# Kernel tuning notes

Measured on AMD Instinct MI355X. Metric: run time of the kernel, lower is better.

Reference implementation:

```python
import jax, jax.numpy as jnp
import numpy as np

EPS = 1e-5

def _bn(z, gamma, beta):
    mu = z.mean(axis=0)
    var = z.var(axis=0)  # biased, matches torch BN normalization
    return (z - mu) * jax.lax.rsqrt(var + EPS) * gamma + beta

def _sage_bn_relu(h, src, dst, n_nodes, Wl, bl, Wr, gamma, beta):
    # SAGEConv (mean aggr): out = lin_l(mean_{j in N(i)} h_j) + lin_r(h_i)
    msg = h[src]                                               # [E, d] gather
    agg = jax.ops.segment_sum(msg, dst, num_segments=n_nodes)  # [N, d]
    cnt = jax.ops.segment_sum(jnp.ones((src.shape[0], 1), h.dtype), dst,
                              num_segments=n_nodes)            # [N, 1]
    agg = jnp.where(cnt > 0, agg / jnp.maximum(cnt, 1.0), 0.0)
    out = agg @ Wl.T + bl + h @ Wr.T
    return jax.nn.relu(_bn(out, gamma, beta))

def setup_inputs() -> dict:
    key = jax.random.key(0)
    N, E, d, out_c, L, U = 50000, 800000, 128, 128, 3, 256
    ks = jax.random.split(key, 16)
    s = 1.0 / np.sqrt(d)
    return {
        "x": jax.random.normal(ks[0], (N, d), jnp.float32),
        "edge_index": jax.random.randint(ks[1], (2, E), 0, N, jnp.int64),
        "atom_mask": jax.random.uniform(ks[2], (N, 1), jnp.float32),
        "u_index": jax.random.randint(ks[3], (U,), 0, N, jnp.int64),
        "lin_l_w": jax.random.uniform(ks[4], (L, d, d), jnp.float32, -s, s),
        "lin_l_b": jax.random.uniform(ks[5], (L, d), jnp.float32, -s, s),
        "lin_r_w": jax.random.uniform(ks[6], (L, d, d), jnp.float32, -s, s),
        "bn_gamma": jnp.ones((L, d), jnp.float32),
        "bn_beta": jnp.zeros((L, d), jnp.float32),
        "ro_w1": jax.random.uniform(ks[7], (d, d), jnp.float32, -s, s),
        "ro_b1": jax.random.uniform(ks[8], (d,), jnp.float32, -s, s),
        "ro_bn_gamma": jnp.ones((d,), jnp.float32),
        "ro_bn_beta": jnp.zeros((d,), jnp.float32),
        "ro_w2": jax.random.uniform(ks[9], (out_c, d), jnp.float32, -s, s),
        "ro_b2": jax.random.uniform(ks[10], (out_c,), jnp.float32, -s, s),
    }

def reference(x, edge_index, atom_mask, u_index, lin_l_w, lin_l_b, lin_r_w,
              bn_gamma, bn_beta, ro_w1, ro_b1, ro_bn_gamma, ro_bn_beta,
              ro_w2, ro_b2):
    N = x.shape[0]
    src, dst = edge_index[0], edge_index[1]
    h = x
    for l in range(lin_l_w.shape[0]):
        h = _sage_bn_relu(h, src, dst, N, lin_l_w[l], lin_l_b[l],
                          lin_r_w[l], bn_gamma[l], bn_beta[l])
    state = h[u_index]                                         # [U, d]
    z = jax.nn.relu(_bn(h @ ro_w1.T + ro_b1, ro_bn_gamma, ro_bn_beta))
    atom = (z @ ro_w2.T + ro_b2) * atom_mask                   # [N, out]
    return (h, atom, state)
```

## Files before the change

### kernel.cpp

```cpp
#include <hip/hip_runtime.h>

#define D 128
#define LDA 136

typedef __attribute__((ext_vector_type(8))) short bf16x8;
typedef __attribute__((ext_vector_type(4))) float f32x4;

__device__ __forceinline__ ushort f2b(float f) {
  union { float f; unsigned u; } a; a.f = f;
  unsigned u = a.u;
  return (ushort)((u + 0x7fffu + ((u >> 16) & 1u)) >> 16);
}
__device__ __forceinline__ float b2f_lo(unsigned v) {
  union { unsigned u; float f; } a; a.u = v << 16; return a.f;
}
__device__ __forceinline__ float b2f_hi(unsigned v) {
  union { unsigned u; float f; } a; a.u = v & 0xffff0000u; return a.f;
}

__global__ void k_prep(const float* __restrict__ x, const float* __restrict__ wl,
                       const float* __restrict__ wr, const float* __restrict__ w1,
                       const float* __restrict__ w2, ushort* __restrict__ hb,
                       ushort* __restrict__ wall, uint4* __restrict__ zr,
                       int nX4, int npX4, int LDD, int nZero4) {
  int i = blockIdx.x * blockDim.x + threadIdx.x;
  if (i < npX4) {
    uint2 pk;
    if (i < nX4) {
      float4 v = *(const float4*)&x[i * 4];
      pk.x = (unsigned)f2b(v.x) | ((unsigned)f2b(v.y) << 16);
      pk.y = (unsigned)f2b(v.z) | ((unsigned)f2b(v.w) << 16);
    } else {
      pk = make_uint2(0u, 0u);
    }
    *(uint2*)&hb[i * 4] = pk;
    return;
  }
  int j = i - npX4;
  int W = 2 * LDD + 2 * D * D;
  if (j < W) {
    float v;
    if (j < LDD) v = wl[j];
    else if (j < 2 * LDD) v = wr[j - LDD];
    else if (j < 2 * LDD + D * D) v = w1[j - 2 * LDD];
    else v = w2[j - 2 * LDD - D * D];
    wall[j] = f2b(v);
    return;
  }
  int z = j - W;
  if (z < nZero4) zr[z] = make_uint4(0u, 0u, 0u, 0u);
}

__global__ void k_histrank(const int* __restrict__ dstI, int* __restrict__ cnt,
                           int* __restrict__ rankdst, int E) {
  int e = blockIdx.x * blockDim.x + threadIdx.x;
  if (e < E) {
    int d = dstI[e];
    int r = atomicAdd(&cnt[d], 1);
    rankdst[e] = (r << 16) | d;
  }
}
__global__ void k_scan1(const int* __restrict__ cnt, int* __restrict__ off,
                        int* __restrict__ bsum, int n) {
  __shared__ int sd[256];
  int t = threadIdx.x;
  int i = blockIdx.x * 256 + t;
  int x = (i < n) ? cnt[i] : 0;
  sd[t] = x;
  __syncthreads();
  for (int s = 1; s < 256; s <<= 1) {
    int v = (t >= s) ? sd[t - s] : 0;
    __syncthreads();
    sd[t] += v;
    __syncthreads();
  }
  if (i < n) off[i] = sd[t] - x;
  if (t == 255) bsum[blockIdx.x] = sd[255];
}
__global__ void k_scan2(const int* __restrict__ bsum, int* __restrict__ boff, int nb) {
  __shared__ int sd[256];
  int t = threadIdx.x;
  int x = (t < nb) ? bsum[t] : 0;
  sd[t] = x;
  __syncthreads();
  for (int s = 1; s < 256; s <<= 1) {
    int v = (t >= s) ? sd[t - s] : 0;
    __syncthreads();
    sd[t] += v;
    __syncthreads();
  }
  if (t < nb) boff[t] = sd[t] - x;
}
__global__ void k_scan3(int* __restrict__ off, const int* __restrict__ boff, int n) {
  int i = blockIdx.x * blockDim.x + threadIdx.x;
  if (i < n) off[i] += boff[i >> 8];
}
__global__ void k_fill(const int* __restrict__ srcI, const int* __restrict__ rankdst,
                       const int* __restrict__ off, ushort* __restrict__ eidx, int E) {
  int e = blockIdx.x * blockDim.x + threadIdx.x;
  if (e < E) {
    int rd = rankdst[e];
    int d = rd & 0xFFFF;
    eidx[off[d] + (rd >> 16)] = (ushort)srcI[e];
  }
}

#define ACC8(A, V, B)                                             \
  A[B + 0] += b2f_lo(V.x); A[B + 1] += b2f_hi(V.x);               \
  A[B + 2] += b2f_lo(V.y); A[B + 3] += b2f_hi(V.y);               \
  A[B + 4] += b2f_lo(V.z); A[B + 5] += b2f_hi(V.z);               \
  A[B + 6] += b2f_lo(V.w); A[B + 7] += b2f_hi(V.w);

template <bool AGG>
__global__ __launch_bounds__(512) void k_fused(
    const ushort* __restrict__ hin, const ushort* __restrict__ Wl,
    const ushort* __restrict__ Wr, const float* __restrict__ bias,
    const int* __restrict__ off, const ushort* __restrict__ eidx,
    ushort* __restrict__ pre, float* __restrict__ sums, int N, int E) {
  __shared__ ushort aggS[128 * LDA];
  __shared__ float ls[2 * D];
  int t = threadIdx.x;
  int r0 = blockIdx.x * 128;

  if (t < 2 * D) ls[t] = 0.f;

  if (AGG) {
    int lrow = t >> 2;
    int row = r0 + lrow;
    int sub = (t & 3) << 3;
    int start = 0, end = 0;
    if (row < N) { start = off[row]; end = (row == N - 1) ? E : off[row + 1]; }
    int deg = end - start;
    float inv = (deg > 0) ? 1.0f / (float)deg : 0.f;
#pragma unroll
    for (int ph = 0; ph < 4; ++ph) {
      const ushort* hbase = hin + ph * 32 + sub;
      float a[8];
#pragma unroll
      for (int i = 0; i < 8; ++i) a[i] = 0.f;
#pragma unroll 2
      for (int e = start; e < end; ++e) {
        int sn = eidx[e];
        uint4 v = *(const uint4*)(hbase + (size_t)sn * D);
        ACC8(a, v, 0)
      }
      uint4 o;
      o.x = (unsigned)f2b(a[0] * inv) | ((unsigned)f2b(a[1] * inv) << 16);
      o.y = (unsigned)f2b(a[2] * inv) | ((unsigned)f2b(a[3] * inv) << 16);
      o.z = (unsigned)f2b(a[4] * inv) | ((unsigned)f2b(a[5] * inv) << 16);
      o.w = (unsigned)f2b(a[6] * inv) | ((unsigned)f2b(a[7] * inv) << 16);
      *(uint4*)&aggS[lrow * LDA + ph * 32 + sub] = o;
    }
  }
  __syncthreads();

  int lane = t & 63;
  int wid = t >> 6;
  int wr = wid >> 1, wc = wid & 1;
  int rw = wr * 32, cw = wc * 64;
  int lr = lane & 15, lk = (lane >> 4) * 8;

  f32x4 acc[2][4];
#pragma unroll
  for (int i = 0; i < 2; ++i)
#pragma unroll
    for (int j = 0; j < 4; ++j) acc[i][j] = (f32x4){0.f, 0.f, 0.f, 0.f};

#pragma unroll
  for (int ks = 0; ks < 4; ++ks) {
    int kb = ks * 32 + lk;
    bf16x8 aA[2], aB[2];
#pragma unroll
    for (int rt = 0; rt < 2; ++rt) {
      if (AGG) {
        aA[rt] = *(const bf16x8*)&aggS[(rw + rt * 16 + lr) * LDA + kb];
        aB[rt] = *(const bf16x8*)&hin[(size_t)(r0 + rw + rt * 16 + lr) * D + kb];
      } else {
        aA[rt] = *(const bf16x8*)&hin[(size_t)(r0 + rw + rt * 16 + lr) * D + kb];
      }
    }
#pragma unroll
    for (int jt = 0; jt < 4; ++jt) {
      bf16x8 b1 = *(const bf16x8*)&Wl[(size_t)(cw + jt * 16 + lr) * D + kb];
      acc[0][jt] = __builtin_amdgcn_mfma_f32_16x16x32_bf16(aA[0], b1, acc[0][jt], 0, 0, 0);
      acc[1][jt] = __builtin_amdgcn_mfma_f32_16x16x32_bf16(aA[1], b1, acc[1][jt], 0, 0, 0);
      if (AGG) {
        bf16x8 b2 = *(const bf16x8*)&Wr[(size_t)(cw + jt * 16 + lr) * D + kb];
        acc[0][jt] = __builtin_amdgcn_mfma_f32_16x16x32_bf16(aB[0], b2, acc[0][jt], 0, 0, 0);
        acc[1][jt] = __builtin_amdgcn_mfma_f32_16x16x32_bf16(aB[1], b2, acc[1][jt], 0, 0, 0);
      }
    }
  }

  int crow = (lane >> 4) * 4;
#pragma unroll
  for (int jt = 0; jt < 4; ++jt) {
    int col = cw + jt * 16 + lr;
    float bv = bias[col];
    float s1 = 0.f, s2 = 0.f;
#pragma unroll
    for (int rt = 0; rt < 2; ++rt) {
      int rbase = r0 + rw + rt * 16 + crow;
#pragma unroll
      for (int rg = 0; rg < 4; ++rg) {
        int row = rbase + rg;
        if (row < N) {
          float v = acc[rt][jt][rg] + bv;
          pre[(size_t)row * D + col] = f2b(v);
          s1 += v; s2 += v * v;
        }
      }
    }
    s1 += __shfl_xor(s1, 16, 64); s1 += __shfl_xor(s1, 32, 64);
    s2 += __shfl_xor(s2, 16, 64); s2 += __shfl_xor(s2, 32, 64);
    if (lane < 16) {
      atomicAdd(&ls[cw + jt * 16 + lane], s1);
      atomicAdd(&ls[D + cw + jt * 16 + lane], s2);
    }
  }
  __syncthreads();
  if (t < 2 * D) atomicAdd(&sums[t], ls[t]);
}

template <bool F32OUT>
__global__ void k_bnrelu(const ushort* __restrict__ pre, const float* __restrict__ sums,
                         const float* __restrict__ gamma, const float* __restrict__ beta,
                         float* __restrict__ fout, ushort* __restrict__ bout,
                         int N, int Np, float invN) {
  int i4 = blockIdx.x * blockDim.x + threadIdx.x;
  if (i4 >= Np * (D / 4)) return;
  int row = i4 >> 5;
  int c4 = (i4 & 31) * 4;
  uint2 pk;
  if (row < N) {
    uint2 pv = *(const uint2*)&pre[(size_t)row * D + c4];
    float4 v = make_float4(b2f_lo(pv.x), b2f_hi(pv.x), b2f_lo(pv.y), b2f_hi(pv.y));
    float4 s = *(const float4*)&sums[c4];
    float4 q = *(const float4*)&sums[D + c4];
    float4 g = *(const float4*)&gamma[c4];
    float4 b = *(const float4*)&beta[c4];
    float mu, var, sc, sh;
    mu = s.x * invN; var = fmaxf(q.x * invN - mu * mu, 0.f);
    sc = g.x * rsqrtf(var + 1e-5f); sh = b.x - mu * sc;
    v.x = fmaxf(fmaf(v.x, sc, sh), 0.f);
    mu = s.y * invN; var = fmaxf(q.y * invN - mu * mu, 0.f);
    sc = g.y * rsqrtf(var + 1e-5f); sh = b.y - mu * sc;
    v.y = fmaxf(fmaf(v.y, sc, sh), 0.f);
    mu = s.z * invN; var = fmaxf(q.z * invN - mu * mu, 0.f);
    sc = g.z * rsqrtf(var + 1e-5f); sh = b.z - mu * sc;
    v.z = fmaxf(fmaf(v.z, sc, sh), 0.f);
    mu = s.w * invN; var = fmaxf(q.w * invN - mu * mu, 0.f);
    sc = g.w * rsqrtf(var + 1e-5f); sh = b.w - mu * sc;
    v.w = fmaxf(fmaf(v.w, sc, sh), 0.f);
    if (F32OUT) *(float4*)&fout[(size_t)row * D + c4] = v;
    pk.x = (unsigned)f2b(v.x) | ((unsigned)f2b(v.y) << 16);
    pk.y = (unsigned)f2b(v.z) | ((unsigned)f2b(v.w) << 16);
  } else {
    pk = make_uint2(0u, 0u);
  }
  *(uint2*)&bout[(size_t)row * D + c4] = pk;
}

__global__ __launch_bounds__(256) void k_mmfin(
    const ushort* __restrict__ A, const ushort* __restrict__ W,
    const float* __restrict__ bias, const float* __restrict__ mask,
    float* __restrict__ out, int N) {
  int t = threadIdx.x;
  int lane = t & 63;
  int wid = t >> 6;
  int wr = wid >> 1, wc = wid & 1;
  int r0 = blockIdx.x * 128 + wr * 64;
  int c0 = wc * 64;
  int lr = lane & 15, lk = (lane >> 4) * 8;

  f32x4 acc[4][4];
#pragma unroll
  for (int i = 0; i < 4; ++i)
#pragma unroll
    for (int j = 0; j < 4; ++j) acc[i][j] = (f32x4){0.f, 0.f, 0.f, 0.f};

#pragma unroll
  for (int ks = 0; ks < 4; ++ks) {
    int kb = ks * 32 + lk;
    bf16x8 a1[4];
#pragma unroll
    for (int rt = 0; rt < 4; ++rt)
      a1[rt] = *(const bf16x8*)&A[(size_t)(r0 + rt * 16 + lr) * D + kb];
#pragma unroll
    for (int jt = 0; jt < 4; ++jt) {
      bf16x8 b1 = *(const bf16x8*)&W[(size_t)(c0 + jt * 16 + lr) * D + kb];
#pragma unroll
      for (int rt = 0; rt < 4; ++rt)
        acc[rt][jt] = __builtin_amdgcn_mfma_f32_16x16x32_bf16(a1[rt], b1, acc[rt][jt], 0, 0, 0);
    }
  }

  int crow = (lane >> 4) * 4;
#pragma unroll
  for (int rt = 0; rt < 4; ++rt) {
    int rbase = r0 + rt * 16 + crow;
#pragma unroll
    for (int jt = 0; jt < 4; ++jt) {
      int col = c0 + jt * 16 + lr;
      float bv = bias[col];
#pragma unroll
      for (int rg = 0; rg < 4; ++rg) {
        int row = rbase + rg;
        if (row < N) {
          float m = mask[row];
          out[(size_t)row * D + col] = (acc[rt][jt][rg] + bv) * m;
        }
      }
    }
  }
}

__global__ void k_gather(const float* __restrict__ h, const int* __restrict__ uidx,
                         float* __restrict__ outp, int U) {
  int u = blockIdx.x;
  int t = threadIdx.x;
  int s = uidx[u];
  *(float4*)&outp[(size_t)u * D + t * 4] = *(const float4*)&h[(size_t)s * D + t * 4];
}

extern "C" void kernel_launch(void* const* d_in, const int* in_sizes, int n_in,
                              void* d_out, int out_size, void* d_ws, size_t ws_size,
                              hipStream_t stream) {
  const float* x        = (const float*)d_in[0];
  const int*   edge     = (const int*)d_in[1];
  const float* amask    = (const float*)d_in[2];
  const int*   uindex   = (const int*)d_in[3];
  const float* lin_l_w  = (const float*)d_in[4];
  const float* lin_l_b  = (const float*)d_in[5];
  const float* lin_r_w  = (const float*)d_in[6];
  const float* bn_gamma = (const float*)d_in[7];
  const float* bn_beta  = (const float*)d_in[8];
  const float* ro_w1    = (const float*)d_in[9];
  const float* ro_b1    = (const float*)d_in[10];
  const float* ro_bng   = (const float*)d_in[11];
  const float* ro_bnb   = (const float*)d_in[12];
  const float* ro_w2    = (const float*)d_in[13];
  const float* ro_b2    = (const float*)d_in[14];

  const int N = in_sizes[0] / D;
  const int E = in_sizes[1] / 2;
  const int U = in_sizes[3];
  const int L = in_sizes[4] / (D * D);
  const int Np = ((N + 127) / 128) * 128;
  const int LDD = L * D * D;

  const int* srcI = edge;
  const int* dstI = edge + E;

  float* outH     = (float*)d_out;
  float* outAtom  = outH + (size_t)N * D;
  float* outState = outAtom + (size_t)N * D;

  char* w = (char*)d_ws;
  ushort* hb   = (ushort*)w; w += (size_t)Np * D * 2;
  ushort* pre  = (ushort*)w; w += (size_t)Np * D * 2;
  ushort* wall = (ushort*)w; w += (size_t)(2 * LDD + 2 * D * D) * 2;
  int*    cnt  = (int*)w;    w += (size_t)N * 4;
  float*  sums = (float*)w;  w += 4 * 2 * D * 4;
  int* off     = (int*)w;    w += (size_t)N * 4;
  int* rankdst = (int*)w;    w += (size_t)E * 4;
  ushort* eidx = (ushort*)w; w += (size_t)((E + 1) & ~1) * 2;
  int* bsum    = (int*)w;    w += 1024;
  int* boff    = (int*)w;    w += 1024;

  ushort* wlb = wall;
  ushort* wrb = wlb + (size_t)LDD;
  ushort* w1b = wrb + (size_t)LDD;
  ushort* w2b = w1b + (size_t)D * D;

  const float invN = 1.0f / (float)N;

  {
    int nX4 = N * D / 4, npX4 = Np * D / 4;
    int W = 2 * LDD + 2 * D * D;
    int nZero4 = (N + 4 * 2 * D) / 4;
    int total = npX4 + W + nZero4;
    k_prep<<<(total + 255) / 256, 256, 0, stream>>>(x, lin_l_w, lin_r_w, ro_w1, ro_w2,
                                                    hb, wall, (uint4*)cnt, nX4, npX4, LDD, nZero4);
  }

  int nbE = (E + 255) / 256;
  int nbN = (N + 255) / 256;
  k_histrank<<<nbE, 256, 0, stream>>>(dstI, cnt, rankdst, E);
  k_scan1<<<nbN, 256, 0, stream>>>(cnt, off, bsum, N);
  k_scan2<<<1, 256, 0, stream>>>(bsum, boff, nbN);
  k_scan3<<<nbN, 256, 0, stream>>>(off, boff, N);
  k_fill<<<nbE, 256, 0, stream>>>(srcI, rankdst, off, eidx, E);

  const int fusedBlocks = Np / 128;
  const int bnBlocks = (Np * (D / 4) + 255) / 256;

  for (int l = 0; l < L; ++l) {
    float* lsums = sums + (size_t)l * 2 * D;
    k_fused<true><<<fusedBlocks, 512, 0, stream>>>(
        hb, wlb + (size_t)l * D * D, wrb + (size_t)l * D * D,
        lin_l_b + (size_t)l * D, off, eidx, pre, lsums, N, E);
    if (l == L - 1)
      k_bnrelu<true><<<bnBlocks, 256, 0, stream>>>(pre, lsums, bn_gamma + (size_t)l * D,
                                                   bn_beta + (size_t)l * D, outH, hb, N, Np, invN);
    else
      k_bnrelu<false><<<bnBlocks, 256, 0, stream>>>(pre, lsums, bn_gamma + (size_t)l * D,
                                                    bn_beta + (size_t)l * D, nullptr, hb, N, Np, invN);
  }

  float* rsums = sums + (size_t)L * 2 * D;
  k_fused<false><<<fusedBlocks, 512, 0, stream>>>(
      hb, w1b, nullptr, ro_b1, off, eidx, pre, rsums, N, E);
  k_bnrelu<false><<<bnBlocks, 256, 0, stream>>>(pre, rsums, ro_bng, ro_bnb, nullptr, hb, N, Np, invN);
  k_mmfin<<<Np / 128, 256, 0, stream>>>(hb, w2b, ro_b2, amask, outAtom, N);
  k_gather<<<U, 32, 0, stream>>>(outH, uindex, outState, U);
}
```

Measured before the change: 365.9 us.

## Widen fused SAGE kernel to 1024 threads with LDS-staged edge indices

The fused aggregate+GEMM kernel now runs 1024 threads per block. Each block first stages its edge source indices into shared memory (capped at 3072, with a global-memory fallback). Each node row is then gathered by 8 threads, each handling 16 features in a single pass, instead of 4 threads making four 32-feature passes. The MFMA stage is split over 16 waves with 32 columns each. The intent is more memory-level parallelism in the gather and fewer reloads of the edge-index list, at the cost of more registers per thread and a stricter occupancy bound.

```diff
diff --git a/kernel.cpp b/kernel.cpp
--- a/kernel.cpp
+++ b/kernel.cpp
@@ -2,6 +2,7 @@
 
 #define D 128
 #define LDA 136
+#define ECAP 3072
 
 typedef __attribute__((ext_vector_type(8))) short bf16x8;
 typedef __attribute__((ext_vector_type(4))) float f32x4;
@@ -112,12 +113,13 @@
   A[B + 6] += b2f_lo(V.w); A[B + 7] += b2f_hi(V.w);
 
 template <bool AGG>
-__global__ __launch_bounds__(512) void k_fused(
+__global__ __launch_bounds__(1024, 8) void k_fused(
     const ushort* __restrict__ hin, const ushort* __restrict__ Wl,
     const ushort* __restrict__ Wr, const float* __restrict__ bias,
     const int* __restrict__ off, const ushort* __restrict__ eidx,
     ushort* __restrict__ pre, float* __restrict__ sums, int N, int E) {
   __shared__ ushort aggS[128 * LDA];
+  __shared__ ushort eidxS[ECAP];
   __shared__ float ls[2 * D];
   int t = threadIdx.x;
   int r0 = blockIdx.x * 128;
@@ -125,46 +127,61 @@
   if (t < 2 * D) ls[t] = 0.f;
 
   if (AGG) {
-    int lrow = t >> 2;
+    int eBase = off[r0];
+    int eEnd = (r0 + 128 < N) ? off[r0 + 128] : E;
+    int cnt = eEnd - eBase;
+    for (int i = t; i < cnt && i < ECAP; i += 1024) eidxS[i] = eidx[eBase + i];
+    __syncthreads();
+
+    int lrow = t >> 3;
     int row = r0 + lrow;
-    int sub = (t & 3) << 3;
+    int part = (t & 7) << 4;
+    float a[16];
+#pragma unroll
+    for (int i = 0; i < 16; ++i) a[i] = 0.f;
     int start = 0, end = 0;
     if (row < N) { start = off[row]; end = (row == N - 1) ? E : off[row + 1]; }
-    int deg = end - start;
-    float inv = (deg > 0) ? 1.0f / (float)deg : 0.f;
-#pragma unroll
-    for (int ph = 0; ph < 4; ++ph) {
-      const ushort* hbase = hin + ph * 32 + sub;
-      float a[8];
-#pragma unroll
-      for (int i = 0; i < 8; ++i) a[i] = 0.f;
+    const ushort* hbase = hin + part;
+    if (cnt <= ECAP) {
+#pragma unroll 4
+      for (int e = start; e < end; ++e) {
+        int sn = eidxS[e - eBase];
+        const uint4* p = (const uint4*)(hbase + (size_t)sn * D);
+        uint4 v0 = p[0], v1 = p[1];
+        ACC8(a, v0, 0) ACC8(a, v1, 8)
+      }
+    } else {
 #pragma unroll 2
       for (int e = start; e < end; ++e) {
         int sn = eidx[e];
-        uint4 v = *(const uint4*)(hbase + (size_t)sn * D);
-        ACC8(a, v, 0)
-      }
-      uint4 o;
-      o.x = (unsigned)f2b(a[0] * inv) | ((unsigned)f2b(a[1] * inv) << 16);
-      o.y = (unsigned)f2b(a[2] * inv) | ((unsigned)f2b(a[3] * inv) << 16);
-      o.z = (unsigned)f2b(a[4] * inv) | ((unsigned)f2b(a[5] * inv) << 16);
-      o.w = (unsigned)f2b(a[6] * inv) | ((unsigned)f2b(a[7] * inv) << 16);
-      *(uint4*)&aggS[lrow * LDA + ph * 32 + sub] = o;
-    }
+        const uint4* p = (const uint4*)(hbase + (size_t)sn * D);
+        uint4 v0 = p[0], v1 = p[1];
+        ACC8(a, v0, 0) ACC8(a, v1, 8)
+      }
+    }
+    int deg = end - start;
+    float inv = (deg > 0) ? 1.0f / (float)deg : 0.f;
+    unsigned o[8];
+#pragma unroll
+    for (int i = 0; i < 8; ++i)
+      o[i] = (unsigned)f2b(a[2 * i] * inv) | ((unsigned)f2b(a[2 * i + 1] * inv) << 16);
+    uint4* dst = (uint4*)&aggS[lrow * LDA + part];
+    dst[0] = make_uint4(o[0], o[1], o[2], o[3]);
+    dst[1] = make_uint4(o[4], o[5], o[6], o[7]);
   }
   __syncthreads();
 
   int lane = t & 63;
   int wid = t >> 6;
-  int wr = wid >> 1, wc = wid & 1;
-  int rw = wr * 32, cw = wc * 64;
+  int wr = wid >> 2, wc = wid & 3;
+  int rw = wr * 32, cw = wc * 32;
   int lr = lane & 15, lk = (lane >> 4) * 8;
 
-  f32x4 acc[2][4];
+  f32x4 acc[2][2];
 #pragma unroll
   for (int i = 0; i < 2; ++i)
 #pragma unroll
-    for (int j = 0; j < 4; ++j) acc[i][j] = (f32x4){0.f, 0.f, 0.f, 0.f};
+    for (int j = 0; j < 2; ++j) acc[i][j] = (f32x4){0.f, 0.f, 0.f, 0.f};
 
 #pragma unroll
   for (int ks = 0; ks < 4; ++ks) {
@@ -180,7 +197,7 @@
       }
     }
 #pragma unroll
-    for (int jt = 0; jt < 4; ++jt) {
+    for (int jt = 0; jt < 2; ++jt) {
       bf16x8 b1 = *(const bf16x8*)&Wl[(size_t)(cw + jt * 16 + lr) * D + kb];
       acc[0][jt] = __builtin_amdgcn_mfma_f32_16x16x32_bf16(aA[0], b1, acc[0][jt], 0, 0, 0);
       acc[1][jt] = __builtin_amdgcn_mfma_f32_16x16x32_bf16(aA[1], b1, acc[1][jt], 0, 0, 0);
@@ -194,7 +211,7 @@
 
   int crow = (lane >> 4) * 4;
 #pragma unroll
-  for (int jt = 0; jt < 4; ++jt) {
+  for (int jt = 0; jt < 2; ++jt) {
     int col = cw + jt * 16 + lr;
     float bv = bias[col];
     float s1 = 0.f, s2 = 0.f;
@@ -397,7 +414,7 @@
 
   for (int l = 0; l < L; ++l) {
     float* lsums = sums + (size_t)l * 2 * D;
-    k_fused<true><<<fusedBlocks, 512, 0, stream>>>(
+    k_fused<true><<<fusedBlocks, 1024, 0, stream>>>(
         hb, wlb + (size_t)l * D * D, wrb + (size_t)l * D * D,
         lin_l_b + (size_t)l * D, off, eidx, pre, lsums, N, E);
     if (l == L - 1)
@@ -409,7 +426,7 @@
   }
 
   float* rsums = sums + (size_t)L * 2 * D;
-  k_fused<false><<<fusedBlocks, 512, 0, stream>>>(
+  k_fused<false><<<fusedBlocks, 1024, 0, stream>>>(
       hb, w1b, nullptr, ro_b1, off, eidx, pre, rsums, N, E);
   k_bnrelu<false><<<bnBlocks, 256, 0, stream>>>(pre, rsums, ro_bng, ro_bnb, nullptr, hb, N, Np, invN);
   k_mmfin<<<Np / 128, 256, 0, stream>>>(hb, w2b, ro_b2, amask, outAtom, N);
```

New measurement: 387.4 us. +5.9%, slower.

## Split fused aggregation+GEMM into separate column-sliced aggregation and GEMM kernels

Applied to the files above, without the earlier changes.

The neighbour mean-aggregation moves out of the fused GEMM kernel into its own kernel. That kernel launches four times as many blocks, each handling one 32-column slice for 128 rows, and writes the bf16 aggregate to a new global buffer. The GEMM kernel then reads both operands from global memory. The aim is more parallelism and latency hiding for the irregular gather, which was serialized over four phases per thread and limited occupancy through shared-memory use. The cost is an extra global write and read of the aggregate, one more launch per layer, and repeated edge-index reads for each slice.

```diff
diff --git a/kernel.cpp b/kernel.cpp
--- a/kernel.cpp
+++ b/kernel.cpp
@@ -1,7 +1,6 @@
 #include <hip/hip_runtime.h>
 
 #define D 128
-#define LDA 136
 
 typedef __attribute__((ext_vector_type(8))) short bf16x8;
 typedef __attribute__((ext_vector_type(4))) float f32x4;
@@ -111,47 +110,51 @@
   A[B + 4] += b2f_lo(V.z); A[B + 5] += b2f_hi(V.z);               \
   A[B + 6] += b2f_lo(V.w); A[B + 7] += b2f_hi(V.w);
 
-template <bool AGG>
-__global__ __launch_bounds__(512) void k_fused(
-    const ushort* __restrict__ hin, const ushort* __restrict__ Wl,
-    const ushort* __restrict__ Wr, const float* __restrict__ bias,
-    const int* __restrict__ off, const ushort* __restrict__ eidx,
-    ushort* __restrict__ pre, float* __restrict__ sums, int N, int E) {
-  __shared__ ushort aggS[128 * LDA];
+__global__ __launch_bounds__(512) void k_aggslice(
+    const ushort* __restrict__ hin, const int* __restrict__ off,
+    const ushort* __restrict__ eidx, ushort* __restrict__ aggb,
+    int N, int E) {
+  int b = blockIdx.x;
+  int s = b & 3;
+  int t = threadIdx.x;
+  int lrow = t >> 2;
+  int row = (b >> 2) * 128 + lrow;
+  int col = s * 32 + ((t & 3) << 3);
+  ushort* dst = &aggb[(size_t)row * D + col];
+  if (row >= N) { *(uint4*)dst = make_uint4(0u, 0u, 0u, 0u); return; }
+  int start = off[row];
+  int end = (row == N - 1) ? E : off[row + 1];
+  float a[8];
+#pragma unroll
+  for (int i = 0; i < 8; ++i) a[i] = 0.f;
+  const ushort* hbase = hin + col;
+#pragma unroll 2
+  for (int e = start; e < end; ++e) {
+    int sn = eidx[e];
+    uint4 v = *(const uint4*)(hbase + (size_t)sn * D);
+    ACC8(a, v, 0)
+  }
+  int deg = end - start;
+  float inv = (deg > 0) ? 1.0f / (float)deg : 0.f;
+  uint4 o;
+  o.x = (unsigned)f2b(a[0] * inv) | ((unsigned)f2b(a[1] * inv) << 16);
+  o.y = (unsigned)f2b(a[2] * inv) | ((unsigned)f2b(a[3] * inv) << 16);
+  o.z = (unsigned)f2b(a[4] * inv) | ((unsigned)f2b(a[5] * inv) << 16);
+  o.w = (unsigned)f2b(a[6] * inv) | ((unsigned)f2b(a[7] * inv) << 16);
+  *(uint4*)dst = o;
+}
+
+template <bool DUAL>
+__global__ __launch_bounds__(512) void k_mm(
+    const ushort* __restrict__ A1, const ushort* __restrict__ A2,
+    const ushort* __restrict__ Wl, const ushort* __restrict__ Wr,
+    const float* __restrict__ bias, ushort* __restrict__ pre,
+    float* __restrict__ sums, int N) {
   __shared__ float ls[2 * D];
   int t = threadIdx.x;
   int r0 = blockIdx.x * 128;
 
   if (t < 2 * D) ls[t] = 0.f;
-
-  if (AGG) {
-    int lrow = t >> 2;
-    int row = r0 + lrow;
-    int sub = (t & 3) << 3;
-    int start = 0, end = 0;
-    if (row < N) { start = off[row]; end = (row == N - 1) ? E : off[row + 1]; }
-    int deg = end - start;
-    float inv = (deg > 0) ? 1.0f / (float)deg : 0.f;
-#pragma unroll
-    for (int ph = 0; ph < 4; ++ph) {
-      const ushort* hbase = hin + ph * 32 + sub;
-      float a[8];
-#pragma unroll
-      for (int i = 0; i < 8; ++i) a[i] = 0.f;
-#pragma unroll 2
-      for (int e = start; e < end; ++e) {
-        int sn = eidx[e];
-        uint4 v = *(const uint4*)(hbase + (size_t)sn * D);
-        ACC8(a, v, 0)
-      }
-      uint4 o;
-      o.x = (unsigned)f2b(a[0] * inv) | ((unsigned)f2b(a[1] * inv) << 16);
-      o.y = (unsigned)f2b(a[2] * inv) | ((unsigned)f2b(a[3] * inv) << 16);
-      o.z = (unsigned)f2b(a[4] * inv) | ((unsigned)f2b(a[5] * inv) << 16);
-      o.w = (unsigned)f2b(a[6] * inv) | ((unsigned)f2b(a[7] * inv) << 16);
-      *(uint4*)&aggS[lrow * LDA + ph * 32 + sub] = o;
-    }
-  }
   __syncthreads();
 
   int lane = t & 63;
@@ -172,19 +175,15 @@
     bf16x8 aA[2], aB[2];
 #pragma unroll
     for (int rt = 0; rt < 2; ++rt) {
-      if (AGG) {
-        aA[rt] = *(const bf16x8*)&aggS[(rw + rt * 16 + lr) * LDA + kb];
-        aB[rt] = *(const bf16x8*)&hin[(size_t)(r0 + rw + rt * 16 + lr) * D + kb];
-      } else {
-        aA[rt] = *(const bf16x8*)&hin[(size_t)(r0 + rw + rt * 16 + lr) * D + kb];
-      }
+      aA[rt] = *(const bf16x8*)&A1[(size_t)(r0 + rw + rt * 16 + lr) * D + kb];
+      if (DUAL) aB[rt] = *(const bf16x8*)&A2[(size_t)(r0 + rw + rt * 16 + lr) * D + kb];
     }
 #pragma unroll
     for (int jt = 0; jt < 4; ++jt) {
       bf16x8 b1 = *(const bf16x8*)&Wl[(size_t)(cw + jt * 16 + lr) * D + kb];
       acc[0][jt] = __builtin_amdgcn_mfma_f32_16x16x32_bf16(aA[0], b1, acc[0][jt], 0, 0, 0);
       acc[1][jt] = __builtin_amdgcn_mfma_f32_16x16x32_bf16(aA[1], b1, acc[1][jt], 0, 0, 0);
-      if (AGG) {
+      if (DUAL) {
         bf16x8 b2 = *(const bf16x8*)&Wr[(size_t)(cw + jt * 16 + lr) * D + kb];
         acc[0][jt] = __builtin_amdgcn_mfma_f32_16x16x32_bf16(aB[0], b2, acc[0][jt], 0, 0, 0);
         acc[1][jt] = __builtin_amdgcn_mfma_f32_16x16x32_bf16(aB[1], b2, acc[1][jt], 0, 0, 0);
@@ -358,6 +357,7 @@
 
   char* w = (char*)d_ws;
   ushort* hb   = (ushort*)w; w += (size_t)Np * D * 2;
+  ushort* aggb = (ushort*)w; w += (size_t)Np * D * 2;
   ushort* pre  = (ushort*)w; w += (size_t)Np * D * 2;
   ushort* wall = (ushort*)w; w += (size_t)(2 * LDD + 2 * D * D) * 2;
   int*    cnt  = (int*)w;    w += (size_t)N * 4;
@@ -392,14 +392,16 @@
   k_scan3<<<nbN, 256, 0, stream>>>(off, boff, N);
   k_fill<<<nbE, 256, 0, stream>>>(srcI, rankdst, off, eidx, E);
 
-  const int fusedBlocks = Np / 128;
+  const int mmBlocks = Np / 128;
+  const int aggBlocks = mmBlocks * 4;
   const int bnBlocks = (Np * (D / 4) + 255) / 256;
 
   for (int l = 0; l < L; ++l) {
     float* lsums = sums + (size_t)l * 2 * D;
-    k_fused<true><<<fusedBlocks, 512, 0, stream>>>(
-        hb, wlb + (size_t)l * D * D, wrb + (size_t)l * D * D,
-        lin_l_b + (size_t)l * D, off, eidx, pre, lsums, N, E);
+    k_aggslice<<<aggBlocks, 512, 0, stream>>>(hb, off, eidx, aggb, N, E);
+    k_mm<true><<<mmBlocks, 512, 0, stream>>>(
+        aggb, hb, wlb + (size_t)l * D * D, wrb + (size_t)l * D * D,
+        lin_l_b + (size_t)l * D, pre, lsums, N);
     if (l == L - 1)
       k_bnrelu<true><<<bnBlocks, 256, 0, stream>>>(pre, lsums, bn_gamma + (size_t)l * D,
                                                    bn_beta + (size_t)l * D, outH, hb, N, Np, invN);
@@ -409,9 +411,9 @@
   }
 
   float* rsums = sums + (size_t)L * 2 * D;
-  k_fused<false><<<fusedBlocks, 512, 0, stream>>>(
-      hb, w1b, nullptr, ro_b1, off, eidx, pre, rsums, N, E);
+  k_mm<false><<<mmBlocks, 512, 0, stream>>>(
+      hb, nullptr, w1b, nullptr, ro_b1, pre, rsums, N);
   k_bnrelu<false><<<bnBlocks, 256, 0, stream>>>(pre, rsums, ro_bng, ro_bnb, nullptr, hb, N, Np, invN);
-  k_mmfin<<<Np / 128, 256, 0, stream>>>(hb, w2b, ro_b2, amask, outAtom, N);
+  k_mmfin<<<mmBlocks, 256, 0, stream>>>(hb, w2b, ro_b2, amask, outAtom, N);
   k_gather<<<U, 32, 0, stream>>>(outH, uindex, outState, U);
 }
```

Measured after the change: 373.3 us. +2.0%, slower.
